# Performance work log

Hardware: AMD Instinct MI355X
Metric: run time of the kernel (lower is better)

## Reference

```python
import jax, jax.numpy as jnp
import numpy as np

S = 2048  # expert group size
M = 768   # hidden size
H = 3072  # intermediate size
E = 16    # num experts


def top2_gating(gates):
    # gates: [G, S, E]
    G, S_, E_ = gates.shape
    C = 2 * S_ // E_
    mask_dtype = jnp.int32
    index_1 = jnp.argmax(gates, axis=-1)
    mask_1 = jax.nn.one_hot(index_1, E_, dtype=mask_dtype)
    gate_1 = jnp.einsum('GSE,GSE->GS', gates, mask_1)
    gates_without_top_1 = gates * (1 - mask_1)
    index_2 = jnp.argmax(gates_without_top_1, axis=-1)
    mask_2 = jax.nn.one_hot(index_2, E_, dtype=mask_dtype)
    gate_2 = jnp.einsum('GSE,GSE->GS', gates_without_top_1, mask_2)
    pos_1 = jnp.cumsum(mask_1, axis=-2) - mask_1
    mask_1 = mask_1 * (pos_1 < C)
    pos_1 = jnp.einsum('GSE,GSE->GS', pos_1, mask_1)
    mask_1_count = jnp.sum(mask_1, axis=-2)
    mask_1_flat = jnp.sum(mask_1, axis=-1)
    pos_2 = jnp.cumsum(mask_2, axis=-2) - mask_2 + jnp.expand_dims(mask_1_count, -2)
    mask_2 = mask_2 * (pos_2 < C)
    pos_2 = jnp.einsum('GSE,GSE->GS', pos_2, mask_2)
    mask_2_flat = jnp.sum(mask_2, axis=-1)
    gate_1 = gate_1 * mask_1_flat
    gate_2 = gate_2 * mask_2_flat
    denom = gate_1 + gate_2
    denom = jnp.where(denom > 0, denom, jnp.ones_like(denom))
    gate_1 = gate_1 / denom
    gate_2 = gate_2 / denom
    a = jnp.expand_dims(gate_1 * mask_1_flat, -1) * jax.nn.one_hot(index_1, E_, dtype=gates.dtype)
    b = jax.nn.one_hot(pos_1, C, dtype=gates.dtype)
    first = jnp.einsum('GSE,GSC->GSEC', a, b)
    a = jnp.expand_dims(gate_2 * mask_2_flat, -1) * jax.nn.one_hot(index_2, E_, dtype=gates.dtype)
    b = jax.nn.one_hot(pos_2, C, dtype=gates.dtype)
    second = jnp.einsum('GSE,GSC->GSEC', a, b)
    combined_tensor = first + second
    dispatch_tensor = combined_tensor.astype(jnp.bool_)
    return combined_tensor, dispatch_tensor


def setup_inputs() -> dict:
    key = jax.random.key(0)
    k1, k2, k3, k4 = jax.random.split(key, 4)
    inputs = jax.random.normal(k1, (4, 1024, M), dtype=jnp.float32)
    wg = jax.random.normal(k2, (M, E), dtype=jnp.float32) * (1.0 / np.sqrt(M))
    wi = jax.random.normal(k3, (E, M, H), dtype=jnp.float32) * (1.0 / np.sqrt(M))
    wo = jax.random.normal(k4, (E, H, M), dtype=jnp.float32) * (1.0 / np.sqrt(H))
    return {"inputs": inputs, "wg": wg, "wi": wi, "wo": wo}


def reference(inputs, wg, wi, wo):
    x = jnp.reshape(inputs, (-1, S, M))                      # [G, S, M]
    gates = jax.nn.softmax(jnp.einsum('GSM,ME->GSE', x, wg))
    combined_weights, dispatch_mask = top2_gating(gates)
    dispatched = jnp.einsum('GSEC,GSM->EGCM',
                            dispatch_mask.astype(x.dtype), x)
    h = jnp.einsum('EGCM,EMH->EGCH', dispatched, wi)
    h = jax.nn.relu(h)
    expert_out = jnp.einsum('EGCH,EHM->GECM', h, wo)
    out = jnp.einsum('GSEC,GECM->GSM', combined_weights, expert_out)
    return jnp.reshape(out, inputs.shape)
```

## Files before the change

kernel.cpp:

```cpp
#include <hip/hip_runtime.h>
#include <hip/hip_bf16.h>
#include <cstdint>
#include <cstddef>

#define S_TOK 2048
#define M_DIM 768
#define H_DIM 3072
#define E_NUM 16
#define CAP   256

using s16x8 = __attribute__((ext_vector_type(8))) short;
using f32x4 = __attribute__((ext_vector_type(4))) float;

__device__ __forceinline__ unsigned short f2bf(float f) {
    unsigned u = __float_as_uint(f);
    unsigned r = 0x7fffu + ((u >> 16) & 1u);
    return (unsigned short)((u + r) >> 16);
}

__device__ __forceinline__ void async16(const void* g, void* l) {
    __builtin_amdgcn_global_load_lds((const __attribute__((address_space(1))) void*)g,
                                     (__attribute__((address_space(3))) void*)l, 16, 0, 0);
}

__global__ void gating_kernel(const float* __restrict__ x, const float* __restrict__ wg,
                              int* __restrict__ e1o, int* __restrict__ e2o,
                              float* __restrict__ g1o, float* __restrict__ g2o, int ntok) {
    int gid  = blockIdx.x * blockDim.x + threadIdx.x;
    int tok  = gid >> 6;
    int lane = threadIdx.x & 63;
    if (tok >= ntok) return;
    const float* xr = x + (size_t)tok * M_DIM;
    float acc[E_NUM];
#pragma unroll
    for (int e = 0; e < E_NUM; ++e) acc[e] = 0.f;
    for (int m = lane; m < M_DIM; m += 64) {
        float xv = xr[m];
        const float* wr = wg + (size_t)m * E_NUM;
#pragma unroll
        for (int e = 0; e < E_NUM; ++e) acc[e] += xv * wr[e];
    }
#pragma unroll
    for (int off = 32; off >= 1; off >>= 1) {
#pragma unroll
        for (int e = 0; e < E_NUM; ++e) acc[e] += __shfl_xor(acc[e], off, 64);
    }
    if (lane == 0) {
        float mx = acc[0];
#pragma unroll
        for (int e = 1; e < E_NUM; ++e) mx = fmaxf(mx, acc[e]);
        float p[E_NUM]; float s = 0.f;
#pragma unroll
        for (int e = 0; e < E_NUM; ++e) { p[e] = expf(acc[e] - mx); s += p[e]; }
        float inv = 1.f / s;
        int b1 = 0; float v1 = -1.f;
#pragma unroll
        for (int e = 0; e < E_NUM; ++e) { if (p[e] > v1) { v1 = p[e]; b1 = e; } }
        int b2 = 0; float v2 = -1.f;
#pragma unroll
        for (int e = 0; e < E_NUM; ++e) { if (e != b1 && p[e] > v2) { v2 = p[e]; b2 = e; } }
        e1o[tok] = b1; e2o[tok] = b2;
        g1o[tok] = v1 * inv; g2o[tok] = v2 * inv;
    }
}

__global__ void assign_kernel(const int* __restrict__ e1a, const int* __restrict__ e2a,
                              const float* __restrict__ g1a, const float* __restrict__ g2a,
                              int* __restrict__ slot1, int* __restrict__ slot2,
                              float* __restrict__ w1, float* __restrict__ w2,
                              int* __restrict__ tfs, int G) {
    int g    = blockIdx.x;
    int tid  = threadIdx.x;
    int w    = tid >> 6;
    int lane = tid & 63;
    __shared__ int cnt1s[E_NUM];

    for (int i = tid; i < E_NUM * CAP; i += 1024) tfs[(size_t)g * E_NUM * CAP + i] = -1;
    __syncthreads();

    {
        int cnt = 0;
        for (int base = 0; base < S_TOK; base += 64) {
            int t = g * S_TOK + base + lane;
            bool pred = (e1a[t] == w);
            unsigned long long bal = __ballot(pred);
            int prefix = __popcll(bal & ((1ull << lane) - 1ull));
            if (pred) {
                int pos = cnt + prefix;
                if (pos < CAP) {
                    slot1[t] = w * CAP + pos;
                    tfs[((size_t)g * E_NUM + w) * CAP + pos] = base + lane;
                } else {
                    slot1[t] = -1;
                }
            }
            cnt += __popcll(bal);
        }
        if (lane == 0) cnt1s[w] = cnt < CAP ? cnt : CAP;
    }
    __syncthreads();
    {
        int cnt = cnt1s[w];
        for (int base = 0; base < S_TOK; base += 64) {
            int t = g * S_TOK + base + lane;
            bool pred = (e2a[t] == w);
            unsigned long long bal = __ballot(pred);
            int prefix = __popcll(bal & ((1ull << lane) - 1ull));
            if (pred) {
                int pos = cnt + prefix;
                if (pos < CAP) {
                    slot2[t] = w * CAP + pos;
                    tfs[((size_t)g * E_NUM + w) * CAP + pos] = base + lane;
                } else {
                    slot2[t] = -1;
                }
            }
            cnt += __popcll(bal);
        }
    }
    __syncthreads();
    for (int t = tid; t < S_TOK; t += 1024) {
        int gt = g * S_TOK + t;
        float a = slot1[gt] >= 0 ? g1a[gt] : 0.f;
        float b = slot2[gt] >= 0 ? g2a[gt] : 0.f;
        float denom = a + b;
        if (!(denom > 0.f)) denom = 1.f;
        w1[gt] = a / denom;
        w2[gt] = b / denom;
    }
}

__global__ void convert_x_kernel(const float* __restrict__ x, unsigned short* __restrict__ xb,
                                 int ntok) {
    int i4 = blockIdx.x * blockDim.x + threadIdx.x;
    size_t base = (size_t)i4 * 4;
    size_t n_real = (size_t)ntok * M_DIM;
    size_t n_tot  = (size_t)(ntok + 1) * M_DIM;
    if (base >= n_tot) return;
    ushort4 o;
    if (base < n_real) {
        float4 v = *(const float4*)&x[base];
        o.x = f2bf(v.x); o.y = f2bf(v.y); o.z = f2bf(v.z); o.w = f2bf(v.w);
    } else {
        o.x = o.y = o.z = o.w = 0;
    }
    *(ushort4*)&xb[base] = o;
}

__global__ __launch_bounds__(256) void transpose_conv_kernel(const float* __restrict__ src,
                                                             unsigned short* __restrict__ dst,
                                                             int R, int C) {
    __shared__ float T[64][65];
    int e  = blockIdx.z;
    int c0 = blockIdx.x * 64;
    int r0 = blockIdx.y * 64;
    int tid = threadIdx.x;
    int lx = tid & 63, ly = tid >> 6;
    const float* Sp = src + (size_t)e * R * C;
#pragma unroll
    for (int i = 0; i < 16; ++i) {
        int r = i * 4 + ly;
        T[r][lx] = Sp[(size_t)(r0 + r) * C + c0 + lx];
    }
    __syncthreads();
    unsigned short* D = dst + (size_t)e * C * R;
    int rb = (tid & 15) * 4;
    int cy = tid >> 4;
#pragma unroll
    for (int p = 0; p < 4; ++p) {
        int c = p * 16 + cy;
        ushort4 o;
        o.x = f2bf(T[rb + 0][c]);
        o.y = f2bf(T[rb + 1][c]);
        o.z = f2bf(T[rb + 2][c]);
        o.w = f2bf(T[rb + 3][c]);
        *(ushort4*)&D[(size_t)(c0 + c) * R + r0 + rb] = o;
    }
}

template<int KLEN, bool GATHER>
__global__ __launch_bounds__(256) void mfma_gemm_kernel(
        const unsigned short* __restrict__ A,
        const unsigned short* __restrict__ B,
        const int* __restrict__ tfs,
        void* __restrict__ Out, int G, int N_total) {
    __shared__ unsigned short As[128 * 32];
    __shared__ unsigned short Bs[128 * 32];
    __shared__ int rowtok[128];

    int NB  = gridDim.x;
    int bid = blockIdx.x;
    int lid = bid;
    if ((NB & 7) == 0) {
        int per = NB >> 3;
        lid = (bid & 7) * per + (bid >> 3);
    }
    int NT_N = N_total >> 7;
    int c  = lid & 1;
    int r1 = lid >> 1;
    int g  = r1 % G;
    int r2 = r1 / G;
    int n  = r2 % NT_N;
    int e  = r2 / NT_N;
    int z  = e * G + g;
    int n0 = n * 128;
    int c0 = c * 128;
    int tid = threadIdx.x;

    if (GATHER) {
        if (tid < 128) rowtok[tid] = tfs[((size_t)g * E_NUM + e) * CAP + c0 + tid];
        __syncthreads();
    }

    int r4 = tid >> 2, l4 = tid & 3;
    const unsigned short *apt0, *apt1;
    if (GATHER) {
        int t0 = rowtok[r4], t1 = rowtok[64 + r4];
        size_t row0 = (t0 < 0) ? (size_t)(G * S_TOK) : (size_t)(g * S_TOK + t0);
        size_t row1 = (t1 < 0) ? (size_t)(G * S_TOK) : (size_t)(g * S_TOK + t1);
        apt0 = A + row0 * KLEN + l4 * 8;
        apt1 = A + row1 * KLEN + l4 * 8;
    } else {
        apt0 = A + ((size_t)z * CAP + c0 + r4) * KLEN + l4 * 8;
        apt1 = apt0 + (size_t)64 * KLEN;
    }
    const unsigned short* Bexp = B + (size_t)e * N_total * KLEN;
    const unsigned short* bpt0 = Bexp + ((size_t)n0 + r4) * KLEN + l4 * 8;
    const unsigned short* bpt1 = bpt0 + (size_t)64 * KLEN;

    int wv = tid >> 6;
    unsigned short* as0 = &As[(wv * 16) * 32];
    unsigned short* as1 = &As[(64 + wv * 16) * 32];
    unsigned short* bs0 = &Bs[(wv * 16) * 32];
    unsigned short* bs1 = &Bs[(64 + wv * 16) * 32];

    int lane = tid & 63;
    int r = lane & 15, q = lane >> 4;
    int wm = wv & 1, wn = wv >> 1;

    f32x4 acc[4][4];
#pragma unroll
    for (int i = 0; i < 4; ++i)
#pragma unroll
        for (int j = 0; j < 4; ++j) acc[i][j] = (f32x4)(0.f);

    for (int k0 = 0; k0 < KLEN; k0 += 32) {
        async16(apt0, as0);
        async16(apt1, as1);
        async16(bpt0, bs0);
        async16(bpt1, bs1);
        apt0 += 32; apt1 += 32; bpt0 += 32; bpt1 += 32;
        __syncthreads();
        s16x8 af[4], bfr[4];
#pragma unroll
        for (int i = 0; i < 4; ++i)
            af[i] = *(const s16x8*)&As[(wm * 64 + i * 16 + r) * 32 + q * 8];
#pragma unroll
        for (int j = 0; j < 4; ++j)
            bfr[j] = *(const s16x8*)&Bs[(wn * 64 + j * 16 + r) * 32 + q * 8];
#pragma unroll
        for (int i = 0; i < 4; ++i)
#pragma unroll
            for (int j = 0; j < 4; ++j)
                acc[i][j] = __builtin_amdgcn_mfma_f32_16x16x32_bf16(af[i], bfr[j], acc[i][j], 0, 0, 0);
        __syncthreads();
    }

    if (GATHER) {
        unsigned short* H = (unsigned short*)Out;
#pragma unroll
        for (int i = 0; i < 4; ++i) {
#pragma unroll
            for (int v = 0; v < 4; ++v) {
                int m_loc = wm * 64 + i * 16 + q * 4 + v;
                unsigned short* row = H + ((size_t)z * CAP + c0 + m_loc) * N_total + n0;
#pragma unroll
                for (int j = 0; j < 4; ++j) {
                    int n_loc = wn * 64 + j * 16 + r;
                    row[n_loc] = f2bf(fmaxf(acc[i][j][v], 0.f));
                }
            }
        }
    } else {
        float* O = (float*)Out;
#pragma unroll
        for (int i = 0; i < 4; ++i) {
#pragma unroll
            for (int v = 0; v < 4; ++v) {
                int m_loc = wm * 64 + i * 16 + q * 4 + v;
                float* row = O + (((size_t)g * E_NUM + e) * CAP + c0 + m_loc) * N_total + n0;
#pragma unroll
                for (int j = 0; j < 4; ++j) {
                    int n_loc = wn * 64 + j * 16 + r;
                    row[n_loc] = acc[i][j][v];
                }
            }
        }
    }
}

__global__ void combine_kernel(const float* __restrict__ eo,
                               const int* __restrict__ slot1, const int* __restrict__ slot2,
                               const float* __restrict__ w1, const float* __restrict__ w2,
                               float* __restrict__ out, int G) {
    int t = blockIdx.x;
    int g = t / S_TOK;
    int tid = threadIdx.x;
    int s1 = slot1[t], s2 = slot2[t];
    float a = w1[t], b = w2[t];
    const float* base_g = eo + (size_t)g * E_NUM * CAP * M_DIM;
    const float* p1 = base_g + (size_t)(s1 < 0 ? 0 : s1) * M_DIM;
    const float* p2 = base_g + (size_t)(s2 < 0 ? 0 : s2) * M_DIM;
    for (int m = tid; m < M_DIM; m += 256) {
        float v = 0.f;
        if (s1 >= 0) v += a * p1[m];
        if (s2 >= 0) v += b * p2[m];
        out[(size_t)t * M_DIM + m] = v;
    }
}

extern "C" void kernel_launch(void* const* d_in, const int* in_sizes, int n_in,
                              void* d_out, int out_size, void* d_ws, size_t ws_size,
                              hipStream_t stream) {
    const float* x  = (const float*)d_in[0];
    const float* wg = (const float*)d_in[1];
    const float* wi = (const float*)d_in[2];
    const float* wo = (const float*)d_in[3];
    float* out = (float*)d_out;

    int ntok = in_sizes[0] / M_DIM;
    int G = ntok / S_TOK;

    char* wsp = (char*)d_ws;
    auto carve = [&](size_t bytes) {
        void* p = (void*)wsp;
        wsp += (bytes + 255) & ~(size_t)255;
        return p;
    };
    int*   e1    = (int*)carve((size_t)ntok * 4);
    int*   e2    = (int*)carve((size_t)ntok * 4);
    float* g1    = (float*)carve((size_t)ntok * 4);
    float* g2    = (float*)carve((size_t)ntok * 4);
    int*   slot1 = (int*)carve((size_t)ntok * 4);
    int*   slot2 = (int*)carve((size_t)ntok * 4);
    float* w1    = (float*)carve((size_t)ntok * 4);
    float* w2    = (float*)carve((size_t)ntok * 4);
    int*   tfs   = (int*)carve((size_t)G * E_NUM * CAP * 4);
    unsigned short* xb  = (unsigned short*)carve((size_t)(ntok + 1) * M_DIM * 2);
    unsigned short* wiT = (unsigned short*)carve((size_t)E_NUM * H_DIM * M_DIM * 2);
    unsigned short* woT = (unsigned short*)carve((size_t)E_NUM * M_DIM * H_DIM * 2);
    unsigned short* h   = (unsigned short*)carve((size_t)E_NUM * G * CAP * H_DIM * 2);
    float* eo = (float*)carve((size_t)G * E_NUM * CAP * M_DIM * 4);

    gating_kernel<<<(ntok * 64 + 255) / 256, 256, 0, stream>>>(x, wg, e1, e2, g1, g2, ntok);
    assign_kernel<<<G, 1024, 0, stream>>>(e1, e2, g1, g2, slot1, slot2, w1, w2, tfs, G);

    int nx4 = ((ntok + 1) * M_DIM) / 4;
    convert_x_kernel<<<(nx4 + 255) / 256, 256, 0, stream>>>(x, xb, ntok);
    transpose_conv_kernel<<<dim3(H_DIM / 64, M_DIM / 64, E_NUM), 256, 0, stream>>>(wi, wiT, M_DIM, H_DIM);
    transpose_conv_kernel<<<dim3(M_DIM / 64, H_DIM / 64, E_NUM), 256, 0, stream>>>(wo, woT, H_DIM, M_DIM);

    mfma_gemm_kernel<M_DIM, true><<<(H_DIM / 128) * (CAP / 128) * E_NUM * G, 256, 0, stream>>>(
        xb, wiT, tfs, h, G, H_DIM);
    mfma_gemm_kernel<H_DIM, false><<<(M_DIM / 128) * (CAP / 128) * E_NUM * G, 256, 0, stream>>>(
        h, woT, tfs, eo, G, M_DIM);

    combine_kernel<<<ntok, 256, 0, stream>>>(eo, slot1, slot2, w1, w2, out, G);
}
```

Measured before the change: 547.0 us.

## Double-buffer GEMM LDS tiles and split-K the second expert GEMM

Adds a two-stage LDS double buffer so the next K tile's async global-to-LDS loads are issued before the current tile's MFMAs, aiming to overlap memory latency with compute. The second GEMM (K=3072) is split into two K halves to double its block count, writing partial outputs into eo and into the now-dead wiT buffer, and the combine kernel sums the two partials. This raises parallelism for the small-grid down projection at the cost of extra fp32 output traffic and combine reads. The double-buffer loop still has one barrier per iteration and no wait before the next stage, so whether loads truly overlap depends on compiler-inserted vmcnt waits.

Result: faster. 535.5 us (-2.1%).

```diff
diff --git a/kernel.cpp b/kernel.cpp
--- a/kernel.cpp
+++ b/kernel.cpp
@@ -178,33 +178,35 @@
     }
 }
 
-template<int KLEN, bool GATHER>
+template<int KLOOP, bool GATHER>
 __global__ __launch_bounds__(256) void mfma_gemm_kernel(
         const unsigned short* __restrict__ A,
         const unsigned short* __restrict__ B,
         const int* __restrict__ tfs,
-        void* __restrict__ Out, int G, int N_total) {
-    __shared__ unsigned short As[128 * 32];
-    __shared__ unsigned short Bs[128 * 32];
+        void* __restrict__ Out0, void* __restrict__ Out1,
+        int G, int N_total, int kstride, int NKH) {
+    __shared__ unsigned short As[2][128 * 32];
+    __shared__ unsigned short Bs[2][128 * 32];
     __shared__ int rowtok[128];
 
     int NB  = gridDim.x;
     int bid = blockIdx.x;
-    int lid = bid;
-    if ((NB & 7) == 0) {
-        int per = NB >> 3;
-        lid = (bid & 7) * per + (bid >> 3);
-    }
+    int per = NB >> 3;
+    int lid = (bid & 7) * per + (bid >> 3);
+
     int NT_N = N_total >> 7;
     int c  = lid & 1;
     int r1 = lid >> 1;
     int g  = r1 % G;
     int r2 = r1 / G;
     int n  = r2 % NT_N;
-    int e  = r2 / NT_N;
+    int r3 = r2 / NT_N;
+    int kh = r3 % NKH;
+    int e  = r3 / NKH;
     int z  = e * G + g;
     int n0 = n * 128;
     int c0 = c * 128;
+    int koff = kh * KLOOP;
     int tid = threadIdx.x;
 
     if (GATHER) {
@@ -218,22 +220,17 @@
         int t0 = rowtok[r4], t1 = rowtok[64 + r4];
         size_t row0 = (t0 < 0) ? (size_t)(G * S_TOK) : (size_t)(g * S_TOK + t0);
         size_t row1 = (t1 < 0) ? (size_t)(G * S_TOK) : (size_t)(g * S_TOK + t1);
-        apt0 = A + row0 * KLEN + l4 * 8;
-        apt1 = A + row1 * KLEN + l4 * 8;
+        apt0 = A + row0 * kstride + koff + l4 * 8;
+        apt1 = A + row1 * kstride + koff + l4 * 8;
     } else {
-        apt0 = A + ((size_t)z * CAP + c0 + r4) * KLEN + l4 * 8;
-        apt1 = apt0 + (size_t)64 * KLEN;
-    }
-    const unsigned short* Bexp = B + (size_t)e * N_total * KLEN;
-    const unsigned short* bpt0 = Bexp + ((size_t)n0 + r4) * KLEN + l4 * 8;
-    const unsigned short* bpt1 = bpt0 + (size_t)64 * KLEN;
+        apt0 = A + ((size_t)z * CAP + c0 + r4) * kstride + koff + l4 * 8;
+        apt1 = apt0 + (size_t)64 * kstride;
+    }
+    const unsigned short* Bexp = B + (size_t)e * N_total * kstride;
+    const unsigned short* bpt0 = Bexp + ((size_t)n0 + r4) * kstride + koff + l4 * 8;
+    const unsigned short* bpt1 = bpt0 + (size_t)64 * kstride;
 
     int wv = tid >> 6;
-    unsigned short* as0 = &As[(wv * 16) * 32];
-    unsigned short* as1 = &As[(64 + wv * 16) * 32];
-    unsigned short* bs0 = &Bs[(wv * 16) * 32];
-    unsigned short* bs1 = &Bs[(64 + wv * 16) * 32];
-
     int lane = tid & 63;
     int r = lane & 15, q = lane >> 4;
     int wm = wv & 1, wn = wv >> 1;
@@ -244,30 +241,39 @@
 #pragma unroll
         for (int j = 0; j < 4; ++j) acc[i][j] = (f32x4)(0.f);
 
-    for (int k0 = 0; k0 < KLEN; k0 += 32) {
-        async16(apt0, as0);
-        async16(apt1, as1);
-        async16(bpt0, bs0);
-        async16(bpt1, bs1);
-        apt0 += 32; apt1 += 32; bpt0 += 32; bpt1 += 32;
-        __syncthreads();
+#define STAGE(b) do {                                    \
+        async16(apt0, &As[b][(wv * 16) * 32]);           \
+        async16(apt1, &As[b][(64 + wv * 16) * 32]);      \
+        async16(bpt0, &Bs[b][(wv * 16) * 32]);           \
+        async16(bpt1, &Bs[b][(64 + wv * 16) * 32]);      \
+        apt0 += 32; apt1 += 32; bpt0 += 32; bpt1 += 32;  \
+    } while (0)
+
+    const int NT = KLOOP / 32;
+    STAGE(0);
+    __syncthreads();
+    int cur = 0;
+    for (int t = 0; t < NT; ++t) {
+        if (t + 1 < NT) STAGE(cur ^ 1);
         s16x8 af[4], bfr[4];
 #pragma unroll
         for (int i = 0; i < 4; ++i)
-            af[i] = *(const s16x8*)&As[(wm * 64 + i * 16 + r) * 32 + q * 8];
+            af[i] = *(const s16x8*)&As[cur][(wm * 64 + i * 16 + r) * 32 + q * 8];
 #pragma unroll
         for (int j = 0; j < 4; ++j)
-            bfr[j] = *(const s16x8*)&Bs[(wn * 64 + j * 16 + r) * 32 + q * 8];
+            bfr[j] = *(const s16x8*)&Bs[cur][(wn * 64 + j * 16 + r) * 32 + q * 8];
 #pragma unroll
         for (int i = 0; i < 4; ++i)
 #pragma unroll
             for (int j = 0; j < 4; ++j)
                 acc[i][j] = __builtin_amdgcn_mfma_f32_16x16x32_bf16(af[i], bfr[j], acc[i][j], 0, 0, 0);
         __syncthreads();
-    }
+        cur ^= 1;
+    }
+#undef STAGE
 
     if (GATHER) {
-        unsigned short* H = (unsigned short*)Out;
+        unsigned short* H = (unsigned short*)Out0;
 #pragma unroll
         for (int i = 0; i < 4; ++i) {
 #pragma unroll
@@ -282,7 +288,7 @@
             }
         }
     } else {
-        float* O = (float*)Out;
+        float* O = (float*)(kh ? Out1 : Out0);
 #pragma unroll
         for (int i = 0; i < 4; ++i) {
 #pragma unroll
@@ -299,7 +305,7 @@
     }
 }
 
-__global__ void combine_kernel(const float* __restrict__ eo,
+__global__ void combine_kernel(const float* __restrict__ eoA, const float* __restrict__ eoB,
                                const int* __restrict__ slot1, const int* __restrict__ slot2,
                                const float* __restrict__ w1, const float* __restrict__ w2,
                                float* __restrict__ out, int G) {
@@ -308,13 +314,15 @@
     int tid = threadIdx.x;
     int s1 = slot1[t], s2 = slot2[t];
     float a = w1[t], b = w2[t];
-    const float* base_g = eo + (size_t)g * E_NUM * CAP * M_DIM;
-    const float* p1 = base_g + (size_t)(s1 < 0 ? 0 : s1) * M_DIM;
-    const float* p2 = base_g + (size_t)(s2 < 0 ? 0 : s2) * M_DIM;
+    size_t gb = (size_t)g * E_NUM * CAP * M_DIM;
+    const float* p1A = eoA + gb + (size_t)(s1 < 0 ? 0 : s1) * M_DIM;
+    const float* p1B = eoB + gb + (size_t)(s1 < 0 ? 0 : s1) * M_DIM;
+    const float* p2A = eoA + gb + (size_t)(s2 < 0 ? 0 : s2) * M_DIM;
+    const float* p2B = eoB + gb + (size_t)(s2 < 0 ? 0 : s2) * M_DIM;
     for (int m = tid; m < M_DIM; m += 256) {
         float v = 0.f;
-        if (s1 >= 0) v += a * p1[m];
-        if (s2 >= 0) v += b * p2[m];
+        if (s1 >= 0) v += a * (p1A[m] + p1B[m]);
+        if (s2 >= 0) v += b * (p2A[m] + p2B[m]);
         out[(size_t)t * M_DIM + m] = v;
     }
 }
@@ -351,6 +359,7 @@
     unsigned short* woT = (unsigned short*)carve((size_t)E_NUM * M_DIM * H_DIM * 2);
     unsigned short* h   = (unsigned short*)carve((size_t)E_NUM * G * CAP * H_DIM * 2);
     float* eo = (float*)carve((size_t)G * E_NUM * CAP * M_DIM * 4);
+    float* eoB = (float*)wiT;
 
     gating_kernel<<<(ntok * 64 + 255) / 256, 256, 0, stream>>>(x, wg, e1, e2, g1, g2, ntok);
     assign_kernel<<<G, 1024, 0, stream>>>(e1, e2, g1, g2, slot1, slot2, w1, w2, tfs, G);
@@ -361,9 +370,9 @@
     transpose_conv_kernel<<<dim3(M_DIM / 64, H_DIM / 64, E_NUM), 256, 0, stream>>>(wo, woT, H_DIM, M_DIM);
 
     mfma_gemm_kernel<M_DIM, true><<<(H_DIM / 128) * (CAP / 128) * E_NUM * G, 256, 0, stream>>>(
-        xb, wiT, tfs, h, G, H_DIM);
-    mfma_gemm_kernel<H_DIM, false><<<(M_DIM / 128) * (CAP / 128) * E_NUM * G, 256, 0, stream>>>(
-        h, woT, tfs, eo, G, M_DIM);
-
-    combine_kernel<<<ntok, 256, 0, stream>>>(eo, slot1, slot2, w1, w2, out, G);
-}
+        xb, wiT, tfs, h, h, G, H_DIM, M_DIM, 1);
+    mfma_gemm_kernel<H_DIM / 2, false><<<(M_DIM / 128) * (CAP / 128) * E_NUM * G * 2, 256, 0, stream>>>(
+        h, woT, tfs, eo, eoB, G, M_DIM, H_DIM, 2);
+
+    combine_kernel<<<ntok, 256, 0, stream>>>(eo, eoB, slot1, slot2, w1, w2, out, G);
+}
```
